# Performance work log

Hardware: AMD Instinct MI355X
Metric: run time of the kernel (lower is better)

Reference implementation:

```python
import jax, jax.numpy as jnp
import numpy as np


def _sobel_filters():
    # fil is the 3x3 smoothing kernel [[1,2,1],[2,4,2],[1,2,1]]
    fil = np.array([[1, 2, 1], [2, 4, 2], [1, 2, 1]], dtype=np.float32)
    fx = np.zeros((3, 3, 3), dtype=np.float32)
    fx[0, :, :] = fil
    fx[2, :, :] = -fil
    fy = np.zeros((3, 3, 3), dtype=np.float32)
    fy[:, 0, :] = fil
    fy[:, 2, :] = -fil
    fz = np.zeros((3, 3, 3), dtype=np.float32)
    fz[:, :, 0] = fil
    fz[:, :, 2] = -fil
    # Stack the three fixed (non-learned) filters as 3 output channels: [O=3, I=1, 3,3,3]
    return jnp.asarray(np.stack([fx, fy, fz])[:, None])


_FILT = _sobel_filters()
_DN = ('NCDHW', 'OIDHW', 'NCDHW')


def _grad3d(v):
    # v: [N,1,D,H,W] -> [N,3,D,H,W], padding=1 == SAME for 3x3x3 stride 1
    return jax.lax.conv_general_dilated(
        v, _FILT.astype(v.dtype), window_strides=(1, 1, 1),
        padding='SAME', dimension_numbers=_DN)


def setup_inputs() -> dict:
    key = jax.random.key(0)
    k1, k2 = jax.random.split(key)
    shape = (2, 1, 160, 192, 224)
    x = jax.random.normal(k1, shape, dtype=jnp.float32)
    y = jax.random.normal(k2, shape, dtype=jnp.float32)
    return {"x": x, "y": y}


def reference(x, y):
    gx = _grad3d(x)  # [N,3,D,H,W]
    gy = _grad3d(y)
    d2 = (gx - gy) ** 2
    # sum over the 3 directions of the per-direction MSE
    return jnp.sum(jnp.mean(d2, axis=(0, 2, 3, 4)))
```

## Files before the change

### kernel.cpp

```cpp
#include <hip/hip_runtime.h>


#define N_  2
#define D_  160
#define H_  192
#define W_  224
#define PS  (H_ * W_)

#define TD   8

constexpr float SCALE = 1.0f / ((float)N_ * D_ * H_ * W_);

__global__ __launch_bounds__(256, 4)
void grad_loss_kernel(const float* __restrict__ x, const float* __restrict__ y,
                      float* __restrict__ out) {
    __shared__ float wsum[4];

    const int tid  = threadIdx.x;
    const int lane = tid & 63;
    const int wv   = tid >> 6;

    const int h  = blockIdx.y * 4 + wv;
    const int nchunks = D_ / TD;
    const int nb = blockIdx.z / nchunks;
    const int d0 = (blockIdx.z % nchunks) * TD;

    const bool wact = lane < 56;
    const int  w0   = lane * 4;

    const float* bx = x + (size_t)nb * ((size_t)D_ * PS);
    const float* by = y + (size_t)nb * ((size_t)D_ * PS);

    bool rok[3];
    int  ro[3];
    #pragma unroll
    for (int r = 0; r < 3; ++r) {
        int hr = h - 1 + r;
        rok[r] = ((unsigned)hr < (unsigned)H_) && wact;
        ro[r]  = hr * W_ + w0;
    }

    const float4 z4 = make_float4(0.f, 0.f, 0.f, 0.f);
    float4 vc[3];
    float4 a0, a1, a2, b0, b1, b2;
    float acc = 0.f;

    {
        const int p = d0 - 1;
        const bool pin = p >= 0;
        #pragma unroll
        for (int r = 0; r < 3; ++r) {
            vc[r] = z4;
            if (pin && rok[r]) {
                const float4 xv = *(const float4*)(bx + p * PS + ro[r]);
                const float4 yv = *(const float4*)(by + p * PS + ro[r]);
                vc[r] = make_float4(xv.x - yv.x, xv.y - yv.y,
                                    xv.z - yv.z, xv.w - yv.w);
            }
        }
    }

    #pragma unroll
    for (int it = 0; it <= TD + 1; ++it) {
        float4 xn[3], yn[3];
        const int p = d0 + it;
        const bool pref = (it <= TD) && (p < D_);
        #pragma unroll
        for (int r = 0; r < 3; ++r) {
            xn[r] = z4; yn[r] = z4;
            if (pref && rok[r]) {
                xn[r] = *(const float4*)(bx + p * PS + ro[r]);
                yn[r] = *(const float4*)(by + p * PS + ro[r]);
            }
        }

        float4 sw[3], gw[3];
        #pragma unroll
        for (int r = 0; r < 3; ++r) {
            float Lm = __shfl_up(vc[r].w, 1, 64);
            float Rp = __shfl_down(vc[r].x, 1, 64);
            if (lane == 0) Lm = 0.f;
            const float4 v = vc[r];
            sw[r] = make_float4(Lm + 2.f * v.x + v.y,
                                v.x + 2.f * v.y + v.z,
                                v.y + 2.f * v.z + v.w,
                                v.z + 2.f * v.w + Rp);
            gw[r] = make_float4(Lm - v.y, v.x - v.z, v.y - v.w, v.z - Rp);
        }
        float4 n0 = make_float4(sw[0].x + 2.f * sw[1].x + sw[2].x,
                                sw[0].y + 2.f * sw[1].y + sw[2].y,
                                sw[0].z + 2.f * sw[1].z + sw[2].z,
                                sw[0].w + 2.f * sw[1].w + sw[2].w);
        float4 n1 = make_float4(sw[0].x - sw[2].x, sw[0].y - sw[2].y,
                                sw[0].z - sw[2].z, sw[0].w - sw[2].w);
        float4 n2 = make_float4(gw[0].x + 2.f * gw[1].x + gw[2].x,
                                gw[0].y + 2.f * gw[1].y + gw[2].y,
                                gw[0].z + 2.f * gw[1].z + gw[2].z,
                                gw[0].w + 2.f * gw[1].w + gw[2].w);

        if (it >= 2 && wact) {
            float4 gx = make_float4(a0.x - n0.x, a0.y - n0.y,
                                    a0.z - n0.z, a0.w - n0.w);
            float4 gy = make_float4(a1.x + 2.f * b1.x + n1.x,
                                    a1.y + 2.f * b1.y + n1.y,
                                    a1.z + 2.f * b1.z + n1.z,
                                    a1.w + 2.f * b1.w + n1.w);
            float4 gz = make_float4(a2.x + 2.f * b2.x + n2.x,
                                    a2.y + 2.f * b2.y + n2.y,
                                    a2.z + 2.f * b2.z + n2.z,
                                    a2.w + 2.f * b2.w + n2.w);
            acc = fmaf(gx.x, gx.x, acc); acc = fmaf(gx.y, gx.y, acc);
            acc = fmaf(gx.z, gx.z, acc); acc = fmaf(gx.w, gx.w, acc);
            acc = fmaf(gy.x, gy.x, acc); acc = fmaf(gy.y, gy.y, acc);
            acc = fmaf(gy.z, gy.z, acc); acc = fmaf(gy.w, gy.w, acc);
            acc = fmaf(gz.x, gz.x, acc); acc = fmaf(gz.y, gz.y, acc);
            acc = fmaf(gz.z, gz.z, acc); acc = fmaf(gz.w, gz.w, acc);
        }

        a0 = b0; a1 = b1; a2 = b2;
        b0 = n0; b1 = n1; b2 = n2;

        #pragma unroll
        for (int r = 0; r < 3; ++r)
            vc[r] = make_float4(xn[r].x - yn[r].x, xn[r].y - yn[r].y,
                                xn[r].z - yn[r].z, xn[r].w - yn[r].w);
    }

    #pragma unroll
    for (int off = 32; off > 0; off >>= 1)
        acc += __shfl_xor(acc, off, 64);
    if (lane == 0) wsum[wv] = acc;
    __syncthreads();
    if (tid == 0) {
        float s = (wsum[0] + wsum[1]) + (wsum[2] + wsum[3]);
        atomicAdd(out, s * SCALE);
    }
}

extern "C" void kernel_launch(void* const* d_in, const int* in_sizes, int n_in,
                              void* d_out, int out_size, void* d_ws, size_t ws_size,
                              hipStream_t stream) {
    const float* x = (const float*)d_in[0];
    const float* y = (const float*)d_in[1];
    float* out = (float*)d_out;

    hipMemsetAsync(out, 0, sizeof(float), stream);

    dim3 block(256);
    dim3 grid(1,
              H_ / 4,
              N_ * (D_ / TD));
    grad_loss_kernel<<<grid, block, 0, stream>>>(x, y, out);
}
```

Baseline: 167.1 us.

## Stage H-tiles in LDS via async global_load_lds with triple-buffered depth pipeline

```diff
diff --git a/kernel.cpp b/kernel.cpp
--- a/kernel.cpp
+++ b/kernel.cpp
@@ -1,4 +1,5 @@
 #include <hip/hip_runtime.h>
+#include <stdint.h>
 
 
 #define N_  2
@@ -7,123 +8,149 @@
 #define W_  224
 #define PS  (H_ * W_)
 
-#define TD   8
-
+#define TD  8
+#define TH  8
+constexpr int SROWS = TH + 2;
+constexpr int RPAD  = 256;
 constexpr float SCALE = 1.0f / ((float)N_ * D_ * H_ * W_);
 
-__global__ __launch_bounds__(256, 4)
+#define DMA16(gp, lp) __builtin_amdgcn_global_load_lds(                        \
+    (const __attribute__((address_space(1))) void*)(gp),                       \
+    (__attribute__((address_space(3))) void*)(lp), 16, 0, 0)
+
+__global__ __launch_bounds__(256, 2)
 void grad_loss_kernel(const float* __restrict__ x, const float* __restrict__ y,
                       float* __restrict__ out) {
+    __shared__ float sbuf[3][SROWS][2][RPAD];
     __shared__ float wsum[4];
 
     const int tid  = threadIdx.x;
     const int lane = tid & 63;
     const int wv   = tid >> 6;
 
-    const int h  = blockIdx.y * 4 + wv;
+    const int h0 = blockIdx.y * TH;
     const int nchunks = D_ / TD;
     const int nb = blockIdx.z / nchunks;
     const int d0 = (blockIdx.z % nchunks) * TD;
 
-    const bool wact = lane < 56;
-    const int  w0   = lane * 4;
+    const float* vbx = x + (size_t)nb * ((size_t)D_ * PS);
+    const float* vby = y + (size_t)nb * ((size_t)D_ * PS);
 
-    const float* bx = x + (size_t)nb * ((size_t)D_ * PS);
-    const float* by = y + (size_t)nb * ((size_t)D_ * PS);
+    const int lo = (lane < 56 ? lane : 55) * 4;
 
-    bool rok[3];
-    int  ro[3];
+    int sl[5], sa[5], srw[5];
+    const float* sb[5];
     #pragma unroll
-    for (int r = 0; r < 3; ++r) {
-        int hr = h - 1 + r;
-        rok[r] = ((unsigned)hr < (unsigned)H_) && wact;
-        ro[r]  = hr * W_ + w0;
+    for (int k = 0; k < 5; ++k) {
+        int item = 5 * wv + k;
+        sl[k] = item >> 1;
+        sa[k] = item & 1;
+        int gh  = h0 - 1 + sl[k];
+        int ghc = min(max(gh, 0), H_ - 1);
+        srw[k] = ghc * W_;
+        sb[k]  = sa[k] ? vby : vbx;
     }
 
+    auto stage = [&](int p, int bsel) {
+        int pc = min(max(p, 0), D_ - 1);
+        size_t poff = (size_t)pc * PS;
+        #pragma unroll
+        for (int k = 0; k < 5; ++k)
+            DMA16(sb[k] + poff + srw[k] + lo, &sbuf[bsel][sl[k]][sa[k]][0]);
+    };
+
+    const bool wact = lane < 56;
+    float rmask[4];
+    #pragma unroll
+    for (int r = 0; r < 4; ++r) {
+        int gh = h0 - 1 + 2 * wv + r;
+        rmask[r] = (((unsigned)gh < (unsigned)H_) && wact) ? 1.f : 0.f;
+    }
+    const int lrd = lane * 4;
+
+    float4 A0[2], A1[2], A2[2], B0[2], B1[2], B2[2];
     const float4 z4 = make_float4(0.f, 0.f, 0.f, 0.f);
-    float4 vc[3];
-    float4 a0, a1, a2, b0, b1, b2;
+    #pragma unroll
+    for (int j = 0; j < 2; ++j) { A0[j]=A1[j]=A2[j]=B0[j]=B1[j]=B2[j]=z4; }
     float acc = 0.f;
 
-    {
-        const int p = d0 - 1;
-        const bool pin = p >= 0;
-        #pragma unroll
-        for (int r = 0; r < 3; ++r) {
-            vc[r] = z4;
-            if (pin && rok[r]) {
-                const float4 xv = *(const float4*)(bx + p * PS + ro[r]);
-                const float4 yv = *(const float4*)(by + p * PS + ro[r]);
-                vc[r] = make_float4(xv.x - yv.x, xv.y - yv.y,
-                                    xv.z - yv.z, xv.w - yv.w);
-            }
-        }
-    }
+    stage(d0 - 1, 0);
+    asm volatile("" ::: "memory");
+    stage(d0, 1);
 
     #pragma unroll
-    for (int it = 0; it <= TD + 1; ++it) {
-        float4 xn[3], yn[3];
-        const int p = d0 + it;
-        const bool pref = (it <= TD) && (p < D_);
+    for (int it = 0; it < TD + 2; ++it) {
+        if (it == TD + 1)
+            asm volatile("s_waitcnt vmcnt(0)\n\ts_barrier" ::: "memory");
+        else
+            asm volatile("s_waitcnt vmcnt(5)\n\ts_barrier" ::: "memory");
+
+        if (it <= TD - 1) stage(d0 + 1 + it, (it + 2) % 3);
+
+        const int q = d0 - 1 + it;
+        const float pm = (q >= 0 && q < D_) ? 1.f : 0.f;
+        const int bsel = it % 3;
+
+        float4 sw[4], gw[4];
         #pragma unroll
-        for (int r = 0; r < 3; ++r) {
-            xn[r] = z4; yn[r] = z4;
-            if (pref && rok[r]) {
-                xn[r] = *(const float4*)(bx + p * PS + ro[r]);
-                yn[r] = *(const float4*)(by + p * PS + ro[r]);
-            }
-        }
-
-        float4 sw[3], gw[3];
-        #pragma unroll
-        for (int r = 0; r < 3; ++r) {
-            float Lm = __shfl_up(vc[r].w, 1, 64);
-            float Rp = __shfl_down(vc[r].x, 1, 64);
+        for (int r = 0; r < 4; ++r) {
+            const int l = 2 * wv + r;
+            const float4 xr = *(const float4*)&sbuf[bsel][l][0][lrd];
+            const float4 yr = *(const float4*)&sbuf[bsel][l][1][lrd];
+            const float m = rmask[r] * pm;
+            float4 v = make_float4((xr.x - yr.x) * m, (xr.y - yr.y) * m,
+                                   (xr.z - yr.z) * m, (xr.w - yr.w) * m);
+            float Lm = __shfl_up(v.w, 1, 64);
+            float Rp = __shfl_down(v.x, 1, 64);
             if (lane == 0) Lm = 0.f;
-            const float4 v = vc[r];
             sw[r] = make_float4(Lm + 2.f * v.x + v.y,
                                 v.x + 2.f * v.y + v.z,
                                 v.y + 2.f * v.z + v.w,
                                 v.z + 2.f * v.w + Rp);
             gw[r] = make_float4(Lm - v.y, v.x - v.z, v.y - v.w, v.z - Rp);
         }
-        float4 n0 = make_float4(sw[0].x + 2.f * sw[1].x + sw[2].x,
-                                sw[0].y + 2.f * sw[1].y + sw[2].y,
-                                sw[0].z + 2.f * sw[1].z + sw[2].z,
-                                sw[0].w + 2.f * sw[1].w + sw[2].w);
-        float4 n1 = make_float4(sw[0].x - sw[2].x, sw[0].y - sw[2].y,
-                                sw[0].z - sw[2].z, sw[0].w - sw[2].w);
-        float4 n2 = make_float4(gw[0].x + 2.f * gw[1].x + gw[2].x,
-                                gw[0].y + 2.f * gw[1].y + gw[2].y,
-                                gw[0].z + 2.f * gw[1].z + gw[2].z,
-                                gw[0].w + 2.f * gw[1].w + gw[2].w);
+        float4 n0[2], n1[2], n2[2];
+        #pragma unroll
+        for (int j = 0; j < 2; ++j) {
+            n0[j] = make_float4(sw[j].x + 2.f * sw[j+1].x + sw[j+2].x,
+                                sw[j].y + 2.f * sw[j+1].y + sw[j+2].y,
+                                sw[j].z + 2.f * sw[j+1].z + sw[j+2].z,
+                                sw[j].w + 2.f * sw[j+1].w + sw[j+2].w);
+            n1[j] = make_float4(sw[j].x - sw[j+2].x, sw[j].y - sw[j+2].y,
+                                sw[j].z - sw[j+2].z, sw[j].w - sw[j+2].w);
+            n2[j] = make_float4(gw[j].x + 2.f * gw[j+1].x + gw[j+2].x,
+                                gw[j].y + 2.f * gw[j+1].y + gw[j+2].y,
+                                gw[j].z + 2.f * gw[j+1].z + gw[j+2].z,
+                                gw[j].w + 2.f * gw[j+1].w + gw[j+2].w);
+        }
 
         if (it >= 2 && wact) {
-            float4 gx = make_float4(a0.x - n0.x, a0.y - n0.y,
-                                    a0.z - n0.z, a0.w - n0.w);
-            float4 gy = make_float4(a1.x + 2.f * b1.x + n1.x,
-                                    a1.y + 2.f * b1.y + n1.y,
-                                    a1.z + 2.f * b1.z + n1.z,
-                                    a1.w + 2.f * b1.w + n1.w);
-            float4 gz = make_float4(a2.x + 2.f * b2.x + n2.x,
-                                    a2.y + 2.f * b2.y + n2.y,
-                                    a2.z + 2.f * b2.z + n2.z,
-                                    a2.w + 2.f * b2.w + n2.w);
-            acc = fmaf(gx.x, gx.x, acc); acc = fmaf(gx.y, gx.y, acc);
-            acc = fmaf(gx.z, gx.z, acc); acc = fmaf(gx.w, gx.w, acc);
-            acc = fmaf(gy.x, gy.x, acc); acc = fmaf(gy.y, gy.y, acc);
-            acc = fmaf(gy.z, gy.z, acc); acc = fmaf(gy.w, gy.w, acc);
-            acc = fmaf(gz.x, gz.x, acc); acc = fmaf(gz.y, gz.y, acc);
-            acc = fmaf(gz.z, gz.z, acc); acc = fmaf(gz.w, gz.w, acc);
+            #pragma unroll
+            for (int j = 0; j < 2; ++j) {
+                float4 gx = make_float4(A0[j].x - n0[j].x, A0[j].y - n0[j].y,
+                                        A0[j].z - n0[j].z, A0[j].w - n0[j].w);
+                float4 gy = make_float4(A1[j].x + 2.f * B1[j].x + n1[j].x,
+                                        A1[j].y + 2.f * B1[j].y + n1[j].y,
+                                        A1[j].z + 2.f * B1[j].z + n1[j].z,
+                                        A1[j].w + 2.f * B1[j].w + n1[j].w);
+                float4 gz = make_float4(A2[j].x + 2.f * B2[j].x + n2[j].x,
+                                        A2[j].y + 2.f * B2[j].y + n2[j].y,
+                                        A2[j].z + 2.f * B2[j].z + n2[j].z,
+                                        A2[j].w + 2.f * B2[j].w + n2[j].w);
+                acc = fmaf(gx.x, gx.x, acc); acc = fmaf(gx.y, gx.y, acc);
+                acc = fmaf(gx.z, gx.z, acc); acc = fmaf(gx.w, gx.w, acc);
+                acc = fmaf(gy.x, gy.x, acc); acc = fmaf(gy.y, gy.y, acc);
+                acc = fmaf(gy.z, gy.z, acc); acc = fmaf(gy.w, gy.w, acc);
+                acc = fmaf(gz.x, gz.x, acc); acc = fmaf(gz.y, gz.y, acc);
+                acc = fmaf(gz.z, gz.z, acc); acc = fmaf(gz.w, gz.w, acc);
+            }
         }
 
-        a0 = b0; a1 = b1; a2 = b2;
-        b0 = n0; b1 = n1; b2 = n2;
-
         #pragma unroll
-        for (int r = 0; r < 3; ++r)
-            vc[r] = make_float4(xn[r].x - yn[r].x, xn[r].y - yn[r].y,
-                                xn[r].z - yn[r].z, xn[r].w - yn[r].w);
+        for (int j = 0; j < 2; ++j) {
+            A0[j] = B0[j]; A1[j] = B1[j]; A2[j] = B2[j];
+            B0[j] = n0[j]; B1[j] = n1[j]; B2[j] = n2[j];
+        }
     }
 
     #pragma unroll
@@ -148,7 +175,7 @@
 
     dim3 block(256);
     dim3 grid(1,
-              H_ / 4,
+              H_ / TH,
               N_ * (D_ / TD));
     grad_loss_kernel<<<grid, block, 0, stream>>>(x, y, out);
 }
```

Result: faster. 138.1 us (-17.4%).
